# Optimization experiments

Hardware: AMD Instinct MI355X
Metric: run time of the kernel (lower is better)

## Reference

```python
import jax, jax.numpy as jnp
import numpy as np

PATCH_NUMS = (1, 2, 4, 8, 16)
BETA = 0.25
A = -0.75  # torch bicubic coefficient


def _cubic(s):
    s = abs(s)
    if s <= 1.0:
        return ((A + 2.0) * s - (A + 3.0)) * s * s + 1.0
    if s < 2.0:
        return (((s - 5.0) * s + 8.0) * s - 4.0) * A
    return 0.0


def bicubic_matrix(n_in, n_out):
    # Row-stochastic 1D resampling matrix matching torch upsample_bicubic2d
    # (align_corners=False: half-pixel centers, border index clamping).
    scale = n_in / n_out
    W = np.zeros((n_out, n_in), dtype=np.float32)
    for i in range(n_out):
        x = (i + 0.5) * scale - 0.5
        x0 = int(np.floor(x))
        t = x - x0
        for off in (-1, 0, 1, 2):
            idx = min(max(x0 + off, 0), n_in - 1)
            W[i, idx] += _cubic(t - off)
    return jnp.asarray(W)


def area_down(x, pn):
    # exact average pooling (h, w divisible by pn)
    b, c, h, w = x.shape
    kh, kw = h // pn, w // pn
    return x.reshape(b, c, pn, kh, pn, kw).mean(axis=(3, 5))


def bicubic_up(x, h_out, w_out):
    b, c, h_in, w_in = x.shape
    Wh = bicubic_matrix(h_in, h_out)  # (h_out, h_in)
    Ww = bicubic_matrix(w_in, w_out)  # (w_out, w_in)
    x = jnp.einsum('Oh,bchw->bcOw', Wh, x)
    x = jnp.einsum('Pw,bchw->bchP', Ww, x)
    return x


def vector_quantize(z, embed, beta):
    # z: (b,c,h,w); embed: (V,c)
    b, c, h, w = z.shape
    zf = z.transpose(0, 2, 3, 1).reshape(-1, c)  # (N,c)
    # squared L2 distances to codebook, (N,V)
    d = (zf * zf).sum(-1, keepdims=True) - 2.0 * zf @ embed.T + (embed * embed).sum(-1)
    idx = jnp.argmin(d, axis=1)  # (N,)
    zq = embed[idx].reshape(b, h, w, c).transpose(0, 3, 1, 2)
    sg = jax.lax.stop_gradient
    loss = beta * jnp.mean((sg(zq) - z) ** 2) + jnp.mean((zq - sg(z)) ** 2)
    zq_st = z + sg(zq - z)  # straight-through estimator
    return zq_st, idx.reshape(b, h, w), loss


def setup_inputs() -> dict:
    key = jax.random.key(0)
    k1, k2 = jax.random.split(key)
    z = jax.random.normal(k1, (256, 32, 16, 16), dtype=jnp.float32)
    embed = jax.random.normal(k2, (4096, 32), dtype=jnp.float32)
    return {"z": z, "embed": embed}


def reference(z, embed):
    b, c, h, w = z.shape
    f_rest = z
    f_hat = jnp.zeros_like(z)
    ms_idx = []
    vq_loss = jnp.float32(0.0)
    n = len(PATCH_NUMS)
    for i, pn in enumerate(PATCH_NUMS):
        z_scale = area_down(f_rest, pn) if i < n - 1 else f_rest
        z_q_scale, idx, loss_i = vector_quantize(z_scale, embed, BETA)
        z_q = bicubic_up(z_q_scale, h, w) if i < n - 1 else z_q_scale
        f_hat = f_hat + z_q
        f_rest = f_rest - z_q
        ms_idx.append(idx)
        vq_loss = vq_loss + loss_i
    vq_loss = vq_loss / n
    return (f_hat, *ms_idx, vq_loss)
```

## Files before the change

### kernel.cpp

```cpp
#include <hip/hip_runtime.h>
#include <hip/hip_bf16.h>
#include <cstdint>
#include <cstddef>


#define B_   256
#define V_   4096
#define NTOT 2097152
#define WIN  128
#define CAP  1024
#define MARGIN_ 1.0f

using bf16x8 = __attribute__((ext_vector_type(8))) short;
using f32x4  = __attribute__((ext_vector_type(4))) float;

__device__ inline short f2bf(float f) {
  __hip_bfloat16 h = __float2bfloat16(f);
  return *reinterpret_cast<short*>(&h);
}
__device__ inline unsigned encf(float f) {
  unsigned u = __float_as_uint(f);
  return (u & 0x80000000u) ? ~u : (u | 0x80000000u);
}
__device__ inline float decf(unsigned u) {
  unsigned b = (u & 0x80000000u) ? (u ^ 0x80000000u) : ~u;
  return __uint_as_float(b);
}
__device__ inline int keyidx(unsigned long long k) {
  int i = (int)(unsigned)(k & 0xffffffffull);
  return min(max(i, 0), V_ - 1);
}
__device__ inline float min3f(float a, float b, float c) {
  float d;
  asm("v_min3_f32 %0, %1, %2, %3" : "=v"(d) : "v"(a), "v"(b), "v"(c));
  return d;
}

__global__ __launch_bounds__(256) void setup_kernel(
    const float* __restrict__ z, const float* __restrict__ embed,
    float* __restrict__ f_rest, float* __restrict__ zrow,
    short* __restrict__ zrowb, short* __restrict__ ebf,
    float* __restrict__ se, float* __restrict__ tables,
    float* __restrict__ loss_slots, unsigned long long* __restrict__ keys0,
    unsigned int* __restrict__ smin0)
{
  const int tid = threadIdx.x;
  const int t = blockIdx.x * 256 + tid;
  float v = z[t];
  f_rest[t] = v;

  __shared__ float sm[256];
  sm[tid] = v;
  __syncthreads();
  if (tid == 0) {
    float s = 0.f;
    for (int i = 0; i < 256; ++i) s += sm[i];
    int c = blockIdx.x & 31, b = blockIdx.x >> 5;
    float val = s * (1.0f / 256.0f);
    zrow[(size_t)b * 32 + c] = val;
    zrowb[(size_t)b * 32 + c] = f2bf(-val);
  }

  if (blockIdx.x < 16) {
    int code = blockIdx.x * 256 + tid;
    float s = 0.f;
#pragma unroll
    for (int c = 0; c < 32; ++c) {
      float e = embed[(size_t)code * 32 + c];
      ebf[(size_t)code * 32 + c] = f2bf(e);
      s += e * e;
    }
    se[code] = s;
  } else if (blockIdx.x == 16) {
    if (tid < 64) {
      int pn_i = tid >> 4;
      int o    = tid & 15;
      int pn   = 1 << pn_i;
      double scale = (double)pn / 16.0;
      double x  = (o + 0.5) * scale - 0.5;
      double x0 = floor(x);
      double tf = x - x0;
      float row[8];
#pragma unroll
      for (int h = 0; h < 8; ++h) row[h] = 0.f;
      const double A = -0.75;
#pragma unroll
      for (int off = -1; off <= 2; ++off) {
        double s = fabs(tf - (double)off);
        double cub;
        if (s <= 1.0)      cub = ((A + 2.0) * s - (A + 3.0)) * s * s + 1.0;
        else if (s < 2.0)  cub = (((s - 5.0) * s + 8.0) * s - 4.0) * A;
        else               cub = 0.0;
        int idx = (int)x0 + off;
        idx = min(max(idx, 0), pn - 1);
        row[idx] = (float)((double)row[idx] + cub);
      }
#pragma unroll
      for (int h = 0; h < 8; ++h) tables[pn_i * 128 + o * 8 + h] = row[h];
    }
  } else if (blockIdx.x == 17) {
    keys0[tid] = ~0ull;
    smin0[tid] = 0xFFFFFFFFu;
  } else if (blockIdx.x >= 20 && blockIdx.x < 60) {
    loss_slots[(blockIdx.x - 20) * 256 + tid] = 0.f;
  }
}

__global__ __launch_bounds__(256) void vq_phaseA_kernel(
    const short* __restrict__ zrowb, const short* __restrict__ ebf,
    const float* __restrict__ se, unsigned int* __restrict__ smin,
    int vchunk)
{
  __shared__ __align__(16) short elds[WIN * 40];
  __shared__ float selds[WIN];

  const int tid = threadIdx.x;
  const int lane = tid & 63, wave = tid >> 6;
  const int col = lane & 15, quad = lane >> 4;
  const int nw = blockIdx.x * 256 + wave * 64;
  const int vbase = blockIdx.y * vchunk;

  bf16x8 af[4];
#pragma unroll
  for (int f = 0; f < 4; ++f)
    af[f] = *(const bf16x8*)(zrowb + (size_t)(nw + f * 16 + col) * 32 + quad * 8);

  float mn[4][4];
#pragma unroll
  for (int f = 0; f < 4; ++f)
#pragma unroll
    for (int r = 0; r < 4; ++r) mn[f][r] = 3.4e38f;

  for (int w0 = 0; w0 < vchunk; w0 += WIN) {
    __syncthreads();
    {
      int row = tid >> 1, half = tid & 1;
      const bf16x8* src = (const bf16x8*)(ebf + (size_t)(vbase + w0 + row) * 32);
      bf16x8* dst = (bf16x8*)(elds + row * 40);
      dst[half * 2]     = src[half * 2];
      dst[half * 2 + 1] = src[half * 2 + 1];
      if (tid < WIN) selds[tid] = 0.5f * se[vbase + w0 + tid];
    }
    __syncthreads();
#pragma unroll 2
    for (int vv = 0; vv < WIN; vv += 32) {
      bf16x8 bfA = *(const bf16x8*)(elds + (vv + col) * 40 + quad * 8);
      bf16x8 bfB = *(const bf16x8*)(elds + (vv + 16 + col) * 40 + quad * 8);
      float sa = selds[vv + col], sb = selds[vv + 16 + col];
      f32x4 cinA = {sa, sa, sa, sa};
      f32x4 cinB = {sb, sb, sb, sb};
      f32x4 da[4], db[4];
#pragma unroll
      for (int f = 0; f < 4; ++f)
        da[f] = __builtin_amdgcn_mfma_f32_16x16x32_bf16(af[f], bfA, cinA, 0, 0, 0);
#pragma unroll
      for (int f = 0; f < 4; ++f)
        db[f] = __builtin_amdgcn_mfma_f32_16x16x32_bf16(af[f], bfB, cinB, 0, 0, 0);
#pragma unroll
      for (int f = 0; f < 4; ++f)
#pragma unroll
        for (int r = 0; r < 4; ++r)
          mn[f][r] = min3f(mn[f][r], da[f][r], db[f][r]);
    }
  }
#pragma unroll
  for (int f = 0; f < 4; ++f)
#pragma unroll
    for (int r = 0; r < 4; ++r) {
      float m = mn[f][r];
      m = fminf(m, __shfl_xor(m, 1, 64));
      m = fminf(m, __shfl_xor(m, 2, 64));
      m = fminf(m, __shfl_xor(m, 4, 64));
      m = fminf(m, __shfl_xor(m, 8, 64));
      mn[f][r] = m;
    }
  if (col == 0) {
#pragma unroll
    for (int f = 0; f < 4; ++f)
#pragma unroll
      for (int r = 0; r < 4; ++r)
        atomicMin(&smin[nw + f * 16 + quad * 4 + r], encf(mn[f][r]));
  }
}

__global__ __launch_bounds__(256) void vq_phaseB_kernel(
    const short* __restrict__ zrowb, const short* __restrict__ ebf,
    const float* __restrict__ se, const unsigned int* __restrict__ smin,
    const float* __restrict__ zrow, const float* __restrict__ embed,
    unsigned long long* __restrict__ keys, int vchunk, int nmax)
{
  __shared__ __align__(16) short elds[WIN * 40];
  __shared__ float selds[WIN];
  __shared__ unsigned long long clist[CAP];
  __shared__ int ccnt;

  const int tid = threadIdx.x;
  const int lane = tid & 63, wave = tid >> 6;
  const int col = lane & 15, quad = lane >> 4;
  const int nw = blockIdx.x * 256 + wave * 64;
  const int vbase = blockIdx.y * vchunk;

  if (tid == 0) ccnt = 0;

  bf16x8 af[4];
#pragma unroll
  for (int f = 0; f < 4; ++f)
    af[f] = *(const bf16x8*)(zrowb + (size_t)(nw + f * 16 + col) * 32 + quad * 8);

  float thr[4][4];
#pragma unroll
  for (int f = 0; f < 4; ++f)
#pragma unroll
    for (int r = 0; r < 4; ++r)
      thr[f][r] = decf(smin[nw + f * 16 + quad * 4 + r]) + MARGIN_;
  float tmax = fmaxf(
      fmaxf(fmaxf(fmaxf(thr[0][0], thr[0][1]), fmaxf(thr[0][2], thr[0][3])),
            fmaxf(fmaxf(thr[1][0], thr[1][1]), fmaxf(thr[1][2], thr[1][3]))),
      fmaxf(fmaxf(fmaxf(thr[2][0], thr[2][1]), fmaxf(thr[2][2], thr[2][3])),
            fmaxf(fmaxf(thr[3][0], thr[3][1]), fmaxf(thr[3][2], thr[3][3]))));

  for (int w0 = 0; w0 < vchunk; w0 += WIN) {
    __syncthreads();
    {
      int row = tid >> 1, half = tid & 1;
      const bf16x8* src = (const bf16x8*)(ebf + (size_t)(vbase + w0 + row) * 32);
      bf16x8* dst = (bf16x8*)(elds + row * 40);
      dst[half * 2]     = src[half * 2];
      dst[half * 2 + 1] = src[half * 2 + 1];
      if (tid < WIN) selds[tid] = 0.5f * se[vbase + w0 + tid];
    }
    __syncthreads();
#pragma unroll 2
    for (int vv = 0; vv < WIN; vv += 32) {
      bf16x8 bfA = *(const bf16x8*)(elds + (vv + col) * 40 + quad * 8);
      bf16x8 bfB = *(const bf16x8*)(elds + (vv + 16 + col) * 40 + quad * 8);
      float sa = selds[vv + col], sb = selds[vv + 16 + col];
      f32x4 cinA = {sa, sa, sa, sa};
      f32x4 cinB = {sb, sb, sb, sb};
      f32x4 da[4], db[4];
#pragma unroll
      for (int f = 0; f < 4; ++f)
        da[f] = __builtin_amdgcn_mfma_f32_16x16x32_bf16(af[f], bfA, cinA, 0, 0, 0);
#pragma unroll
      for (int f = 0; f < 4; ++f)
        db[f] = __builtin_amdgcn_mfma_f32_16x16x32_bf16(af[f], bfB, cinB, 0, 0, 0);
      float m0  = min3f(da[0][0], da[0][1], da[0][2]);
      float m1  = min3f(da[0][3], da[1][0], da[1][1]);
      float m2  = min3f(da[1][2], da[1][3], da[2][0]);
      float m3  = min3f(da[2][1], da[2][2], da[2][3]);
      float m4  = min3f(da[3][0], da[3][1], da[3][2]);
      float m5  = min3f(da[3][3], db[0][0], db[0][1]);
      float m6  = min3f(db[0][2], db[0][3], db[1][0]);
      float m7  = min3f(db[1][1], db[1][2], db[1][3]);
      float m8  = min3f(db[2][0], db[2][1], db[2][2]);
      float m9  = min3f(db[2][3], db[3][0], db[3][1]);
      float m10 = min3f(db[3][2], db[3][3], m0);
      float m11 = min3f(m1, m2, m3);
      float m12 = min3f(m4, m5, m6);
      float m13 = min3f(m7, m8, m9);
      float g   = fminf(min3f(m10, m11, m12), m13);
      if (g <= tmax) {
#pragma unroll
        for (int s = 0; s < 2; ++s) {
#pragma unroll
          for (int f = 0; f < 4; ++f) {
#pragma unroll
            for (int r = 0; r < 4; ++r) {
              float dv = (s == 0) ? da[f][r] : db[f][r];
              if (dv <= thr[f][r]) {
                int n = nw + f * 16 + quad * 4 + r;
                int v = vbase + w0 + vv + s * 16 + col;
                int slot = atomicAdd(&ccnt, 1);
                if (slot < CAP) {
                  clist[slot] =
                      ((unsigned long long)(unsigned)n << 32) | (unsigned)v;
                } else {
                  const float* zp = zrow + (size_t)n * 32;
                  const float* ep = embed + (size_t)v * 32;
                  float dot = 0.f, sz = 0.f;
#pragma unroll 1
                  for (int i = 0; i < 32; ++i) {
                    float zc = zp[i];
                    dot = fmaf(zc, ep[i], dot);
                    sz  = fmaf(zc, zc, sz);
                  }
                  float d = fmaf(-2.0f, dot, sz) + se[v];
                  unsigned long long key =
                      ((unsigned long long)encf(d) << 32) | (unsigned)v;
                  atomicMin(&keys[n], key);
                }
              }
            }
          }
        }
      }
    }
  }

  __syncthreads();
  int tot = min(ccnt, CAP);
  for (int j = tid; j < tot; j += 256) {
    unsigned long long cv = clist[j];
    int n = min((int)(cv >> 32), nmax - 1);
    int v = min((int)(cv & 0xffffffffull), V_ - 1);
    const float* zp = zrow + (size_t)n * 32;
    const float* ep = embed + (size_t)v * 32;
    float dot = 0.f, sz = 0.f;
#pragma unroll
    for (int i = 0; i < 32; ++i) {
      float zc = zp[i];
      dot = fmaf(zc, ep[i], dot);
      sz  = fmaf(zc, zc, sz);
    }
    float d = fmaf(-2.0f, dot, sz) + se[v];
    unsigned long long key =
        ((unsigned long long)encf(d) << 32) | (unsigned)v;
    atomicMin(&keys[n], key);
  }
}

__global__ __launch_bounds__(256) void up_update_kernel(
    const float* __restrict__ embed, const unsigned long long* __restrict__ keys,
    const float* __restrict__ tbl, float* __restrict__ f_rest, int pn,
    float* __restrict__ zrow, short* __restrict__ zrowb,
    unsigned long long* __restrict__ keys_nb, unsigned int* __restrict__ smin_nb,
    int pn_next, int n_next,
    float* __restrict__ idx_out, float* __restrict__ loss_slot)
{
  __shared__ float sm[256];
  __shared__ float sm_e[64];
  const int tid = threadIdx.x;
  const int t = blockIdx.x * 256 + tid;
  const int p = tid & 15, o = tid >> 4;
  const int c = blockIdx.x & 31, b = blockIdx.x >> 5;
  const int pn2 = pn * pn;

  float pre = f_rest[t];
  sm[tid] = pre;
  if (tid < pn2) {
    int idx = keyidx(keys[b * pn2 + tid]);
    if (c == 0) idx_out[b * pn2 + tid] = (float)idx;
    sm_e[tid] = embed[(size_t)idx * 32 + c];
  }
  __syncthreads();

  float lsum = 0.f;
  if (tid < pn2) {
    int k = 16 / pn;
    int ph = tid / pn, pw = tid - ph * pn;
    float s = 0.f;
    for (int i = 0; i < k; ++i)
      for (int j = 0; j < k; ++j)
        s += sm[(ph * k + i) * 16 + (pw * k + j)];
    float zavg = s * (1.0f / (k * k));
    float d = sm_e[tid] - zavg;
    lsum = d * d;
  }
#pragma unroll
  for (int off = 32; off > 0; off >>= 1) lsum += __shfl_down(lsum, off, 64);
  if ((tid & 63) == 0)
    atomicAdd(loss_slot + ((blockIdx.x & 127) << 4), lsum);

  const float* Wo = tbl + o * 8;
  const float* Wp = tbl + p * 8;
  float acc = 0.f;
  for (int w = 0; w < pn; ++w) {
    float inner = 0.f;
    for (int h = 0; h < pn; ++h)
      inner = fmaf(Wo[h], sm_e[h * pn + w], inner);
    acc = fmaf(Wp[w], inner, acc);
  }
  float nr = pre - acc;
  f_rest[t] = nr;

  __syncthreads();
  sm[tid] = nr;
  __syncthreads();
  const int pnn2 = pn_next * pn_next;
  if (tid < pnn2) {
    int ph = tid / pn_next, pw = tid - ph * pn_next;
    int k = 16 / pn_next;
    float s = 0.f;
    for (int i = 0; i < k; ++i)
      for (int j = 0; j < k; ++j)
        s += sm[(ph * k + i) * 16 + (pw * k + j)];
    float zavg = s * (1.0f / (k * k));
    size_t nn = (size_t)(b * pnn2 + tid);
    zrow[nn * 32 + c]  = zavg;
    zrowb[nn * 32 + c] = f2bf(-zavg);
  }
  if (t < n_next) {
    keys_nb[t] = ~0ull;
    smin_nb[t] = 0xFFFFFFFFu;
  }
}

__global__ __launch_bounds__(256) void final_add_kernel(
    const float* __restrict__ z, const float* __restrict__ f_rest,
    const float* __restrict__ embed, const unsigned long long* __restrict__ keys,
    float* __restrict__ f_hat, float* __restrict__ idx_out,
    float* __restrict__ loss_slot)
{
  const int tid = threadIdx.x;
  const int t = blockIdx.x * 256 + tid;
  const int c = blockIdx.x & 31, b = blockIdx.x >> 5;
  const int n = b * 256 + tid;
  int idx = keyidx(keys[n]);
  if (c == 0) idx_out[n] = (float)idx;
  float e = embed[(size_t)idx * 32 + c];
  float fr = f_rest[t];
  f_hat[t] = (z[t] - fr) + e;
  float d = e - fr;
  float lsum = d * d;
#pragma unroll
  for (int off = 32; off > 0; off >>= 1) lsum += __shfl_down(lsum, off, 64);
  if ((tid & 63) == 0)
    atomicAdd(loss_slot + ((blockIdx.x & 127) << 4), lsum);
}

__global__ __launch_bounds__(128) void loss_final_kernel(
    const float* __restrict__ loss_slots, float* __restrict__ out_loss)
{
  __shared__ float lred[2];
  const int tid = threadIdx.x;
  const float numel[5] = {8192.f, 32768.f, 131072.f, 524288.f, 2097152.f};
  float tot = 0.f;
  for (int s = 0; s < 5; ++s) {
    float x = loss_slots[s * 2048 + tid * 16];
#pragma unroll
    for (int off = 32; off > 0; off >>= 1) x += __shfl_down(x, off, 64);
    if ((tid & 63) == 0) lred[tid >> 6] = x;
    __syncthreads();
    if (tid == 0) {
      float m = (lred[0] + lred[1]) / numel[s];
      tot += 0.25f * m + m;
    }
    __syncthreads();
  }
  if (tid == 0) out_loss[0] = tot / 5.f;
}

extern "C" void kernel_launch(void* const* d_in, const int* in_sizes, int n_in,
                              void* d_out, int out_size, void* d_ws, size_t ws_size,
                              hipStream_t stream)
{
  const float* z     = (const float*)d_in[0];
  const float* embed = (const float*)d_in[1];
  float* out = (float*)d_out;
  float* ws  = (float*)d_ws;

  float* f_rest  = ws;
  float* zrow    = ws + 2097152;
  short* zrowb   = (short*)(ws + 4194304);
  short* ebf     = (short*)(ws + 5242880);
  float* se      = ws + 5308416;
  unsigned int* smin0 = (unsigned int*)(ws + 5312512);
  unsigned int* smin1 = (unsigned int*)(ws + 5378048);
  unsigned long long* keys0 = (unsigned long long*)(ws + 5394432);
  unsigned long long* keys1 = (unsigned long long*)(ws + 5525504);
  float* loss_slots = ws + 5558272;
  float* tables     = ws + 5568512;

  unsigned long long* keysb[2] = {keys0, keys1};
  unsigned int*       sminb[2] = {smin0, smin1};

  setup_kernel<<<NTOT / 256, 256, 0, stream>>>(z, embed, f_rest, zrow, zrowb,
                                               ebf, se, tables, loss_slots,
                                               keys0, smin0);

  const int PN[5]  = {1, 2, 4, 8, 16};
  const int NVC[5] = {32, 32, 32, 16, 16};
  int idx_off = NTOT;
  for (int i = 0; i < 5; ++i) {
    int pn = PN[i];
    int N  = B_ * pn * pn;
    int vchunk = V_ / NVC[i];
    unsigned long long* kb = keysb[i & 1];
    unsigned int*       sb = sminb[i & 1];
    dim3 g(N / 256, NVC[i]);
    vq_phaseA_kernel<<<g, 256, 0, stream>>>(zrowb, ebf, se, sb, vchunk);
    vq_phaseB_kernel<<<g, 256, 0, stream>>>(zrowb, ebf, se, sb, zrow, embed,
                                            kb, vchunk, N);
    if (i < 4) {
      int pnn = PN[i + 1];
      up_update_kernel<<<NTOT / 256, 256, 0, stream>>>(
          embed, kb, tables + i * 128, f_rest, pn,
          zrow, zrowb, keysb[(i + 1) & 1], sminb[(i + 1) & 1],
          pnn, B_ * pnn * pnn, out + idx_off, loss_slots + i * 2048);
    } else {
      final_add_kernel<<<NTOT / 256, 256, 0, stream>>>(
          z, f_rest, embed, kb, out, out + idx_off, loss_slots + 4 * 2048);
    }
    idx_off += N;
  }
  loss_final_kernel<<<1, 128, 0, stream>>>(loss_slots, out + 2184448);
}
```

Before: 435.6 us.

## Halve rows per wave in VQ phase kernels to double grid parallelism

Each wave now covers 32 rows (two MFMA fragments) instead of 64, and each block covers 128 rows, so the grid has twice as many blocks along N. The inner loop handles one 16-column codebook tile per iteration rather than two, and the candidate list capacity is halved. Together these cut register and LDS pressure and fill the GPU better at the small early scales (N=256, 1024). The cost is more blocks re-staging the same codebook windows into LDS and less MFMA work per LDS load. A __syncthreads after ccnt initialization is also added.

```diff
diff --git a/kernel.cpp b/kernel.cpp
--- a/kernel.cpp
+++ b/kernel.cpp
@@ -8,7 +8,7 @@
 #define V_   4096
 #define NTOT 2097152
 #define WIN  128
-#define CAP  1024
+#define CAP  512
 #define MARGIN_ 1.0f
 
 using bf16x8 = __attribute__((ext_vector_type(8))) short;
@@ -117,17 +117,17 @@
   const int tid = threadIdx.x;
   const int lane = tid & 63, wave = tid >> 6;
   const int col = lane & 15, quad = lane >> 4;
-  const int nw = blockIdx.x * 256 + wave * 64;
+  const int nw = blockIdx.x * 128 + wave * 32;
   const int vbase = blockIdx.y * vchunk;
 
-  bf16x8 af[4];
-#pragma unroll
-  for (int f = 0; f < 4; ++f)
+  bf16x8 af[2];
+#pragma unroll
+  for (int f = 0; f < 2; ++f)
     af[f] = *(const bf16x8*)(zrowb + (size_t)(nw + f * 16 + col) * 32 + quad * 8);
 
-  float mn[4][4];
-#pragma unroll
-  for (int f = 0; f < 4; ++f)
+  float mn[2][4];
+#pragma unroll
+  for (int f = 0; f < 2; ++f)
 #pragma unroll
     for (int r = 0; r < 4; ++r) mn[f][r] = 3.4e38f;
 
@@ -142,29 +142,20 @@
       if (tid < WIN) selds[tid] = 0.5f * se[vbase + w0 + tid];
     }
     __syncthreads();
-#pragma unroll 2
-    for (int vv = 0; vv < WIN; vv += 32) {
-      bf16x8 bfA = *(const bf16x8*)(elds + (vv + col) * 40 + quad * 8);
-      bf16x8 bfB = *(const bf16x8*)(elds + (vv + 16 + col) * 40 + quad * 8);
-      float sa = selds[vv + col], sb = selds[vv + 16 + col];
-      f32x4 cinA = {sa, sa, sa, sa};
-      f32x4 cinB = {sb, sb, sb, sb};
-      f32x4 da[4], db[4];
-#pragma unroll
-      for (int f = 0; f < 4; ++f)
-        da[f] = __builtin_amdgcn_mfma_f32_16x16x32_bf16(af[f], bfA, cinA, 0, 0, 0);
-#pragma unroll
-      for (int f = 0; f < 4; ++f)
-        db[f] = __builtin_amdgcn_mfma_f32_16x16x32_bf16(af[f], bfB, cinB, 0, 0, 0);
-#pragma unroll
-      for (int f = 0; f < 4; ++f)
-#pragma unroll
-        for (int r = 0; r < 4; ++r)
-          mn[f][r] = min3f(mn[f][r], da[f][r], db[f][r]);
-    }
-  }
-#pragma unroll
-  for (int f = 0; f < 4; ++f)
+    for (int vv = 0; vv < WIN; vv += 16) {
+      bf16x8 bf = *(const bf16x8*)(elds + (vv + col) * 40 + quad * 8);
+      float sevh = selds[vv + col];
+      f32x4 cin = {sevh, sevh, sevh, sevh};
+#pragma unroll
+      for (int f = 0; f < 2; ++f) {
+        f32x4 d = __builtin_amdgcn_mfma_f32_16x16x32_bf16(af[f], bf, cin, 0, 0, 0);
+#pragma unroll
+        for (int r = 0; r < 4; ++r) mn[f][r] = fminf(mn[f][r], d[r]);
+      }
+    }
+  }
+#pragma unroll
+  for (int f = 0; f < 2; ++f)
 #pragma unroll
     for (int r = 0; r < 4; ++r) {
       float m = mn[f][r];
@@ -176,7 +167,7 @@
     }
   if (col == 0) {
 #pragma unroll
-    for (int f = 0; f < 4; ++f)
+    for (int f = 0; f < 2; ++f)
 #pragma unroll
       for (int r = 0; r < 4; ++r)
         atomicMin(&smin[nw + f * 16 + quad * 4 + r], encf(mn[f][r]));
@@ -197,27 +188,26 @@
   const int tid = threadIdx.x;
   const int lane = tid & 63, wave = tid >> 6;
   const int col = lane & 15, quad = lane >> 4;
-  const int nw = blockIdx.x * 256 + wave * 64;
+  const int nw = blockIdx.x * 128 + wave * 32;
   const int vbase = blockIdx.y * vchunk;
 
   if (tid == 0) ccnt = 0;
-
-  bf16x8 af[4];
-#pragma unroll
-  for (int f = 0; f < 4; ++f)
+  __syncthreads();
+
+  bf16x8 af[2];
+#pragma unroll
+  for (int f = 0; f < 2; ++f)
     af[f] = *(const bf16x8*)(zrowb + (size_t)(nw + f * 16 + col) * 32 + quad * 8);
 
-  float thr[4][4];
-#pragma unroll
-  for (int f = 0; f < 4; ++f)
+  float thr[2][4];
+#pragma unroll
+  for (int f = 0; f < 2; ++f)
 #pragma unroll
     for (int r = 0; r < 4; ++r)
       thr[f][r] = decf(smin[nw + f * 16 + quad * 4 + r]) + MARGIN_;
   float tmax = fmaxf(
-      fmaxf(fmaxf(fmaxf(thr[0][0], thr[0][1]), fmaxf(thr[0][2], thr[0][3])),
-            fmaxf(fmaxf(thr[1][0], thr[1][1]), fmaxf(thr[1][2], thr[1][3]))),
-      fmaxf(fmaxf(fmaxf(thr[2][0], thr[2][1]), fmaxf(thr[2][2], thr[2][3])),
-            fmaxf(fmaxf(thr[3][0], thr[3][1]), fmaxf(thr[3][2], thr[3][3]))));
+      fmaxf(fmaxf(thr[0][0], thr[0][1]), fmaxf(thr[0][2], thr[0][3])),
+      fmaxf(fmaxf(thr[1][0], thr[1][1]), fmaxf(thr[1][2], thr[1][3])));
 
   for (int w0 = 0; w0 < vchunk; w0 += WIN) {
     __syncthreads();
@@ -230,65 +220,42 @@
       if (tid < WIN) selds[tid] = 0.5f * se[vbase + w0 + tid];
     }
     __syncthreads();
-#pragma unroll 2
-    for (int vv = 0; vv < WIN; vv += 32) {
-      bf16x8 bfA = *(const bf16x8*)(elds + (vv + col) * 40 + quad * 8);
-      bf16x8 bfB = *(const bf16x8*)(elds + (vv + 16 + col) * 40 + quad * 8);
-      float sa = selds[vv + col], sb = selds[vv + 16 + col];
-      f32x4 cinA = {sa, sa, sa, sa};
-      f32x4 cinB = {sb, sb, sb, sb};
-      f32x4 da[4], db[4];
-#pragma unroll
-      for (int f = 0; f < 4; ++f)
-        da[f] = __builtin_amdgcn_mfma_f32_16x16x32_bf16(af[f], bfA, cinA, 0, 0, 0);
-#pragma unroll
-      for (int f = 0; f < 4; ++f)
-        db[f] = __builtin_amdgcn_mfma_f32_16x16x32_bf16(af[f], bfB, cinB, 0, 0, 0);
-      float m0  = min3f(da[0][0], da[0][1], da[0][2]);
-      float m1  = min3f(da[0][3], da[1][0], da[1][1]);
-      float m2  = min3f(da[1][2], da[1][3], da[2][0]);
-      float m3  = min3f(da[2][1], da[2][2], da[2][3]);
-      float m4  = min3f(da[3][0], da[3][1], da[3][2]);
-      float m5  = min3f(da[3][3], db[0][0], db[0][1]);
-      float m6  = min3f(db[0][2], db[0][3], db[1][0]);
-      float m7  = min3f(db[1][1], db[1][2], db[1][3]);
-      float m8  = min3f(db[2][0], db[2][1], db[2][2]);
-      float m9  = min3f(db[2][3], db[3][0], db[3][1]);
-      float m10 = min3f(db[3][2], db[3][3], m0);
-      float m11 = min3f(m1, m2, m3);
-      float m12 = min3f(m4, m5, m6);
-      float m13 = min3f(m7, m8, m9);
-      float g   = fminf(min3f(m10, m11, m12), m13);
-      if (g <= tmax) {
-#pragma unroll
-        for (int s = 0; s < 2; ++s) {
-#pragma unroll
-          for (int f = 0; f < 4; ++f) {
-#pragma unroll
-            for (int r = 0; r < 4; ++r) {
-              float dv = (s == 0) ? da[f][r] : db[f][r];
-              if (dv <= thr[f][r]) {
-                int n = nw + f * 16 + quad * 4 + r;
-                int v = vbase + w0 + vv + s * 16 + col;
-                int slot = atomicAdd(&ccnt, 1);
-                if (slot < CAP) {
-                  clist[slot] =
-                      ((unsigned long long)(unsigned)n << 32) | (unsigned)v;
-                } else {
-                  const float* zp = zrow + (size_t)n * 32;
-                  const float* ep = embed + (size_t)v * 32;
-                  float dot = 0.f, sz = 0.f;
+    for (int vv = 0; vv < WIN; vv += 16) {
+      bf16x8 bf = *(const bf16x8*)(elds + (vv + col) * 40 + quad * 8);
+      float sevh = selds[vv + col];
+      f32x4 cin = {sevh, sevh, sevh, sevh};
+      f32x4 dd[2];
+      dd[0] = __builtin_amdgcn_mfma_f32_16x16x32_bf16(af[0], bf, cin, 0, 0, 0);
+      dd[1] = __builtin_amdgcn_mfma_f32_16x16x32_bf16(af[1], bf, cin, 0, 0, 0);
+      float a = min3f(dd[0][0], dd[0][1], dd[0][2]);
+      float b = min3f(dd[0][3], dd[1][0], dd[1][1]);
+      float c = min3f(dd[1][2], dd[1][3], a);
+      if (fminf(b, c) <= tmax) {
+#pragma unroll
+        for (int f = 0; f < 2; ++f) {
+#pragma unroll
+          for (int r = 0; r < 4; ++r) {
+            if (dd[f][r] <= thr[f][r]) {
+              int n = nw + f * 16 + quad * 4 + r;
+              int v = vbase + w0 + vv + col;
+              int slot = atomicAdd(&ccnt, 1);
+              if (slot < CAP) {
+                clist[slot] =
+                    ((unsigned long long)(unsigned)n << 32) | (unsigned)v;
+              } else {
+                const float* zp = zrow + (size_t)n * 32;
+                const float* ep = embed + (size_t)v * 32;
+                float dot = 0.f, sz = 0.f;
 #pragma unroll 1
-                  for (int i = 0; i < 32; ++i) {
-                    float zc = zp[i];
-                    dot = fmaf(zc, ep[i], dot);
-                    sz  = fmaf(zc, zc, sz);
-                  }
-                  float d = fmaf(-2.0f, dot, sz) + se[v];
-                  unsigned long long key =
-                      ((unsigned long long)encf(d) << 32) | (unsigned)v;
-                  atomicMin(&keys[n], key);
+                for (int i = 0; i < 32; ++i) {
+                  float zc = zp[i];
+                  dot = fmaf(zc, ep[i], dot);
+                  sz  = fmaf(zc, zc, sz);
                 }
+                float d = fmaf(-2.0f, dot, sz) + se[v];
+                unsigned long long key =
+                    ((unsigned long long)encf(d) << 32) | (unsigned)v;
+                atomicMin(&keys[n], key);
               }
             }
           }
@@ -477,7 +444,7 @@
     int vchunk = V_ / NVC[i];
     unsigned long long* kb = keysb[i & 1];
     unsigned int*       sb = sminb[i & 1];
-    dim3 g(N / 256, NVC[i]);
+    dim3 g(N / 128, NVC[i]);
     vq_phaseA_kernel<<<g, 256, 0, stream>>>(zrowb, ebf, se, sb, vchunk);
     vq_phaseB_kernel<<<g, 256, 0, stream>>>(zrowb, ebf, se, sb, zrow, embed,
                                             kb, vchunk, N);
```

Measured after the change: 396.5 us. -9.0%, faster.
